# Kernel tuning notes

Hardware: AMD Instinct MI355X
Metric: run time of the kernel (lower is better)

The kernel has to match this reference:

```python
import jax, jax.numpy as jnp
import numpy as np

EPS = 1e-5

def binary_activation(x):
    # ReActNet piecewise-polynomial STE: forward = sign(x), grad follows poly
    m1 = (x < -1).astype(x.dtype)
    m2 = (x < 0).astype(x.dtype)
    m3 = (x < 1).astype(x.dtype)
    out1 = -1.0 * m1 + (x * x + 2.0 * x) * (1.0 - m1)
    out2 = out1 * m2 + (-x * x + 2.0 * x) * (1.0 - m2)
    out3 = out2 * m3 + 1.0 * (1.0 - m3)
    return jax.lax.stop_gradient(jnp.sign(x) - out3) + out3

def binary_conv(x, w, stride, padding):
    # per-output-channel scaled sign weights with clamp STE
    scale = jnp.mean(jnp.abs(w), axis=(1, 2, 3), keepdims=True)
    clipped = jnp.clip(w, -1.0, 1.0)
    bw = jax.lax.stop_gradient(scale * jnp.sign(w) - clipped) + clipped
    return jax.lax.conv_general_dilated(
        x, bw, window_strides=(stride, stride),
        padding=[(padding, padding), (padding, padding)],
        dimension_numbers=('NCHW', 'OIHW', 'NCHW'))

def batch_norm(x, g, b):
    mu = jnp.mean(x, axis=(0, 2, 3), keepdims=True)
    var = jnp.mean((x - mu) ** 2, axis=(0, 2, 3), keepdims=True)
    xn = (x - mu) * jax.lax.rsqrt(var + EPS)
    return xn * g[None, :, None, None] + b[None, :, None, None]

def prelu(x, a):
    a = a[None, :, None, None]
    return jnp.where(x >= 0, x, a * x)

def setup_inputs() -> dict:
    key = jax.random.key(0)
    ks = jax.random.split(key, 12)
    N, C, H, W = 32, 256, 56, 56
    d = {
        'x': jax.random.normal(ks[0], (N, C, H, W), jnp.float32),
        'b11': jax.random.normal(ks[1], (1, C, 1, 1), jnp.float32) * 0.1,
        'b12': jax.random.normal(ks[2], (1, C, 1, 1), jnp.float32) * 0.1,
        'b13': jax.random.normal(ks[3], (1, C, 1, 1), jnp.float32) * 0.1,
        'b21': jax.random.normal(ks[4], (1, C, 1, 1), jnp.float32) * 0.1,
        'b22': jax.random.normal(ks[5], (1, C, 1, 1), jnp.float32) * 0.1,
        'b23': jax.random.normal(ks[6], (1, C, 1, 1), jnp.float32) * 0.1,
        'w3x3': jax.random.normal(ks[7], (C, C, 3, 3), jnp.float32) * 0.05,
        'wpw': jax.random.normal(ks[8], (C, C, 1, 1), jnp.float32) * 0.05,
        'g1': jnp.ones((C,), jnp.float32),
        'be1': jnp.zeros((C,), jnp.float32),
        'g2': jnp.ones((C,), jnp.float32),
        'be2': jnp.zeros((C,), jnp.float32),
        'p1': jnp.full((C,), 0.25, jnp.float32),
        'p2': jnp.full((C,), 0.25, jnp.float32),
    }
    return d

def reference(x, b11, b12, b13, b21, b22, b23, w3x3, wpw, g1, be1, g2, be2, p1, p2):
    # stride=1, inplanes == planes branch
    out1 = binary_activation(x + b11)
    out1 = binary_conv(out1, w3x3, stride=1, padding=1)
    out1 = batch_norm(out1, g1, be1)
    out1 = x + out1
    out1 = prelu(out1 + b12, p1) + b13
    out2 = binary_activation(out1 + b21)
    out2 = binary_conv(out2, wpw, stride=1, padding=0)
    out2 = batch_norm(out2, g2, be2)
    out2 = out2 + out1
    out2 = prelu(out2 + b22, p2) + b23
    return out2
```

## Files before the change

### kernel.cpp

```cpp
#include <hip/hip_runtime.h>

typedef __attribute__((ext_vector_type(4))) float  f32x4;
typedef __attribute__((ext_vector_type(8))) short  s16x8;
typedef __attribute__((ext_vector_type(4))) int    i32x4;

#define MFMA16(a, b, c) __builtin_amdgcn_mfma_f32_16x16x32_bf16((a), (b), (c), 0, 0, 0)

__device__ __forceinline__ void gload_lds16(const void* g, void* l) {
  __builtin_amdgcn_global_load_lds((const __attribute__((address_space(1))) void*)g,
                                   (__attribute__((address_space(3))) void*)l, 16, 0, 0);
}

__device__ __forceinline__ unsigned short sgnbits(float v) {
  return v > 0.f ? (unsigned short)0x3F80u : (v < 0.f ? (unsigned short)0xBF80u : (unsigned short)0u);
}

__global__ __launch_bounds__(256) void prep_w(const float* __restrict__ w3,
                                              const float* __restrict__ wpw,
                                              unsigned short* __restrict__ w1s,
                                              unsigned short* __restrict__ w2s,
                                              float* __restrict__ scale1,
                                              float* __restrict__ scale2) {
  const int o = blockIdx.x;
  const int t = threadIdx.x;
  float s = 0.f;
  if (blockIdx.y == 0) {
    for (int u = t; u < 2304; u += 256) {
      int i = u / 9, tap = u % 9;
      float v = w3[(size_t)(o * 256 + i) * 9 + tap];
      s += fabsf(v);
      w1s[(size_t)(tap * 256 + o) * 256 + i] = sgnbits(v);
    }
  } else {
    float v = wpw[o * 256 + t];
    s = fabsf(v);
    w2s[o * 256 + t] = sgnbits(v);
  }
  for (int m = 1; m < 64; m <<= 1) s += __shfl_xor(s, m);
  __shared__ float red[4];
  if ((t & 63) == 0) red[t >> 6] = s;
  __syncthreads();
  if (t == 0) {
    float tot = red[0] + red[1] + red[2] + red[3];
    if (blockIdx.y == 0) scale1[o] = tot / 2304.f;
    else                 scale2[o] = tot / 256.f;
  }
}

__global__ __launch_bounds__(256) void sign_nhwc(const float* __restrict__ x,
                                                 const float* __restrict__ b11,
                                                 unsigned short* __restrict__ out) {
  __shared__ unsigned short l[56 * 256];
  __shared__ float cB[256];
  const int h = blockIdx.x, n = blockIdx.y, t = threadIdx.x;
  cB[t] = b11[t];
  __syncthreads();
  const int wv = t & 15, cg = t >> 4;
  if (wv < 14) {
    const int w0 = wv * 4;
    const int swz = (wv & 7) << 3;
#pragma unroll 4
    for (int it = 0; it < 16; ++it) {
      int c = it * 16 + cg;
      size_t idx = (size_t)(n * 256 + c) * 3136 + h * 56 + w0;
      f32x4 xv = *(const f32x4*)(x + idx);
      float bb = cB[c];
      int cs = c ^ swz;
      l[(w0 + 0) * 256 + cs] = sgnbits(xv[0] + bb);
      l[(w0 + 1) * 256 + cs] = sgnbits(xv[1] + bb);
      l[(w0 + 2) * 256 + cs] = sgnbits(xv[2] + bb);
      l[(w0 + 3) * 256 + cs] = sgnbits(xv[3] + bb);
    }
  }
  __syncthreads();
  unsigned short* op = out + ((size_t)(n * 56 + h) * 56) * 256;
  for (int u = t; u < 56 * 32; u += 256) {
    int w2 = u >> 5, cp = u & 31;
    *(i32x4*)(op + w2 * 256 + cp * 8) =
        *(const i32x4*)&l[w2 * 256 + ((cp * 8) ^ (((w2 >> 2) & 7) << 3))];
  }
}

template <int R>
__global__ __launch_bounds__(256, 2) void conv_bin(const unsigned short* __restrict__ sIn,
                                                   const unsigned short* __restrict__ wSgn,
                                                   float* __restrict__ raw,
                                                   float* __restrict__ S,
                                                   float* __restrict__ SS) {
  constexpr int KD   = 2 * R + 1;
  constexpr int TAPS = KD * KD;
  constexpr int ROWS = 4 + 2 * R;
  constexpr int COLS = 56 + 2 * R;
  __shared__ unsigned short lin[ROWS * COLS * 32];
  __shared__ unsigned short lw[TAPS * 64 * 32];

  const int ot = blockIdx.x, ht = blockIdx.y, n = blockIdx.z;
  const int h0 = ht * 4, oc0 = ot * 64;
  const int t = threadIdx.x;
  const int lane = t & 63, wv = t >> 6;
  const int wm = wv & 1, wn = wv >> 1;
  const int cl = lane & 15, kk = lane >> 4;

  for (int u = t; u < ROWS * COLS * 4; u += 256)
    *(i32x4*)((char*)lin + (size_t)u * 16) = (i32x4){0, 0, 0, 0};

  int bbase[7];
#pragma unroll
  for (int nf = 0; nf < 7; ++nf) {
    int pxl = (wn * 7 + nf) * 16 + cl;
    int r = pxl / 56, c = pxl % 56;
    bbase[nf] = (r * COLS + c) * 64 + kk * 16;
  }
  const int abase = (wm * 32 + cl) * 64 + kk * 16;

  f32x4 acc[2][7];
#pragma unroll
  for (int m = 0; m < 2; ++m)
#pragma unroll
    for (int nf = 0; nf < 7; ++nf) acc[m][nf] = (f32x4){0.f, 0.f, 0.f, 0.f};

  __syncthreads();

  for (int icc = 0; icc < 8; ++icc) {
#pragma unroll
    for (int rr = 0; rr < ROWS; ++rr) {
      int h = h0 - R + rr;
      if (h >= 0 && h < 56 && t < 224) {
        const char* src = (const char*)sIn +
            ((size_t)((n * 56 + h) * 56 + (t >> 2)) * 512 + icc * 64 + (t & 3) * 16);
        char* dst = (char*)lin + ((rr * COLS + R) * 64 + t * 16);
        gload_lds16(src, dst);
      }
    }
    for (int u = t; u < TAPS * 256; u += 256) {
      int tap = u >> 8, rest = u & 255;
      const char* src = (const char*)wSgn +
          ((size_t)(tap * 256 + oc0 + (rest >> 2)) * 512 + icc * 64 + (rest & 3) * 16);
      gload_lds16(src, (char*)lw + (size_t)u * 16);
    }
    __syncthreads();

#pragma unroll
    for (int kh = 0; kh < KD; ++kh)
#pragma unroll
      for (int kw = 0; kw < KD; ++kw) {
        const int tap = kh * KD + kw;
        s16x8 a0 = *(const s16x8*)((const char*)lw + (tap * 4096 + abase));
        s16x8 a1 = *(const s16x8*)((const char*)lw + (tap * 4096 + abase + 1024));
        const int toff = (kh * COLS + kw) * 64;
#pragma unroll
        for (int nf = 0; nf < 7; ++nf) {
          s16x8 b = *(const s16x8*)((const char*)lin + (bbase[nf] + toff));
          acc[0][nf] = MFMA16(a0, b, acc[0][nf]);
          acc[1][nf] = MFMA16(a1, b, acc[1][nf]);
        }
      }
    __syncthreads();
  }

  float sm[2][4], sq[2][4];
#pragma unroll
  for (int m = 0; m < 2; ++m)
#pragma unroll
    for (int r2 = 0; r2 < 4; ++r2) { sm[m][r2] = 0.f; sq[m][r2] = 0.f; }

  const size_t pbase = (size_t)n * 256 * 3136 + (size_t)h0 * 56;
#pragma unroll
  for (int m = 0; m < 2; ++m) {
    const int ocb = oc0 + wm * 32 + m * 16 + kk * 4;
#pragma unroll
    for (int nf = 0; nf < 7; ++nf) {
      const int pxl = (wn * 7 + nf) * 16 + cl;
      f32x4 v = acc[m][nf];
#pragma unroll
      for (int r2 = 0; r2 < 4; ++r2) {
        raw[pbase + (size_t)(ocb + r2) * 3136 + pxl] = v[r2];
        sm[m][r2] += v[r2];
        sq[m][r2] += v[r2] * v[r2];
      }
    }
  }
#pragma unroll
  for (int m = 0; m < 2; ++m)
#pragma unroll
    for (int r2 = 0; r2 < 4; ++r2) {
      float a = sm[m][r2], q = sq[m][r2];
      a += __shfl_xor(a, 1); q += __shfl_xor(q, 1);
      a += __shfl_xor(a, 2); q += __shfl_xor(q, 2);
      a += __shfl_xor(a, 4); q += __shfl_xor(q, 4);
      a += __shfl_xor(a, 8); q += __shfl_xor(q, 8);
      if (cl == 0) {
        int oc = oc0 + wm * 32 + m * 16 + kk * 4 + r2;
        atomicAdd(&S[oc], a);
        atomicAdd(&SS[oc], q);
      }
    }
}

__global__ void bn_coef(const float* __restrict__ S, const float* __restrict__ SS,
                        const float* __restrict__ scale, const float* __restrict__ g,
                        const float* __restrict__ be, const float* __restrict__ bext,
                        float* __restrict__ A, float* __restrict__ B) {
  int o = threadIdx.x;
  const float invN = 1.f / 100352.f;
  float mu_r  = S[o] * invN;
  float var_r = SS[o] * invN - mu_r * mu_r;
  float sc    = scale[o];
  float rstd  = rsqrtf(sc * sc * var_r + 1e-5f);
  A[o] = g[o] * rstd * sc;
  B[o] = be[o] - g[o] * rstd * sc * mu_r + bext[o];
}

__global__ __launch_bounds__(256) void mid_fuse(const float* __restrict__ raw,
                                                const float* __restrict__ x,
                                                const float* __restrict__ A1,
                                                const float* __restrict__ B1,
                                                const float* __restrict__ p1,
                                                const float* __restrict__ b13,
                                                const float* __restrict__ b21,
                                                float* __restrict__ t1,
                                                unsigned short* __restrict__ s2) {
  __shared__ unsigned short l[56 * 256];
  __shared__ float cA[256], cB[256], cP[256], cD[256], cE[256];
  const int h = blockIdx.x, n = blockIdx.y, t = threadIdx.x;
  cA[t] = A1[t]; cB[t] = B1[t]; cP[t] = p1[t]; cD[t] = b13[t]; cE[t] = b21[t];
  __syncthreads();
  const int wv = t & 15, cg = t >> 4;
  if (wv < 14) {
    const int w0 = wv * 4;
    const int swz = (wv & 7) << 3;
#pragma unroll 4
    for (int it = 0; it < 16; ++it) {
      int c = it * 16 + cg;
      size_t idx = (size_t)(n * 256 + c) * 3136 + h * 56 + w0;
      f32x4 xv = *(const f32x4*)(x + idx);
      f32x4 rv = *(const f32x4*)(raw + idx);
      float a = cA[c], b = cB[c], p = cP[c], d = cD[c], e = cE[c];
      f32x4 o;
      int cs = c ^ swz;
#pragma unroll
      for (int j = 0; j < 4; ++j) {
        float u = xv[j] + a * rv[j] + b;
        u = (u >= 0.f ? u : p * u) + d;
        o[j] = u;
        l[(w0 + j) * 256 + cs] = sgnbits(u + e);
      }
      *(f32x4*)(t1 + idx) = o;
    }
  }
  __syncthreads();
  unsigned short* op = s2 + ((size_t)(n * 56 + h) * 56) * 256;
  for (int u = t; u < 56 * 32; u += 256) {
    int w2 = u >> 5, cp = u & 31;
    *(i32x4*)(op + w2 * 256 + cp * 8) =
        *(const i32x4*)&l[w2 * 256 + ((cp * 8) ^ (((w2 >> 2) & 7) << 3))];
  }
}

__global__ __launch_bounds__(256) void final_fuse(const float* __restrict__ raw,
                                                  const float* __restrict__ A2,
                                                  const float* __restrict__ B2,
                                                  const float* __restrict__ p2,
                                                  const float* __restrict__ b23,
                                                  float* out) {
  const int c = blockIdx.x & 255;
  const size_t base = (size_t)blockIdx.x * 3136;
  const float a = A2[c], b = B2[c], p = p2[c], d = b23[c];
  for (int i = threadIdx.x; i < 784; i += 256) {
    f32x4 r  = *(const f32x4*)(raw + base + (size_t)i * 4);
    f32x4 tt = *(const f32x4*)(out + base + (size_t)i * 4);
    f32x4 o;
#pragma unroll
    for (int j = 0; j < 4; ++j) {
      float v = a * r[j] + b + tt[j];
      o[j] = (v >= 0.f ? v : p * v) + d;
    }
    *(f32x4*)(out + base + (size_t)i * 4) = o;
  }
}

extern "C" void kernel_launch(void* const* d_in, const int* in_sizes, int n_in,
                              void* d_out, int out_size, void* d_ws, size_t ws_size,
                              hipStream_t stream) {
  const float* x   = (const float*)d_in[0];
  const float* b11 = (const float*)d_in[1];
  const float* b12 = (const float*)d_in[2];
  const float* b13 = (const float*)d_in[3];
  const float* b21 = (const float*)d_in[4];
  const float* b22 = (const float*)d_in[5];
  const float* b23 = (const float*)d_in[6];
  const float* w3  = (const float*)d_in[7];
  const float* wpw = (const float*)d_in[8];
  const float* g1  = (const float*)d_in[9];
  const float* be1 = (const float*)d_in[10];
  const float* g2  = (const float*)d_in[11];
  const float* be2 = (const float*)d_in[12];
  const float* p1  = (const float*)d_in[13];
  const float* p2  = (const float*)d_in[14];

  char* ws = (char*)d_ws;
  float*          raw    = (float*)(ws);
  unsigned short* sgn    = (unsigned short*)(ws + 102760448);
  unsigned short* w1s    = (unsigned short*)(ws + 154140672);
  unsigned short* w2s    = (unsigned short*)(ws + 155320320);
  float*          scale1 = (float*)(ws + 155451392);
  float*          scale2 = (float*)(ws + 155452416);
  float*          S1     = (float*)(ws + 155453440);
  float*          SS1    = (float*)(ws + 155454464);
  float*          S2     = (float*)(ws + 155455488);
  float*          SS2    = (float*)(ws + 155456512);
  float*          A1     = (float*)(ws + 155457536);
  float*          B1     = (float*)(ws + 155458560);
  float*          A2     = (float*)(ws + 155459584);
  float*          B2     = (float*)(ws + 155460608);
  float*          t1     = (float*)d_out;

  hipMemsetAsync(ws + 155453440, 0, 4096, stream);

  prep_w<<<dim3(256, 2), 256, 0, stream>>>(w3, wpw, w1s, w2s, scale1, scale2);
  sign_nhwc<<<dim3(56, 32), 256, 0, stream>>>(x, b11, sgn);
  conv_bin<1><<<dim3(4, 14, 32), 256, 0, stream>>>(sgn, w1s, raw, S1, SS1);
  bn_coef<<<1, 256, 0, stream>>>(S1, SS1, scale1, g1, be1, b12, A1, B1);
  mid_fuse<<<dim3(56, 32), 256, 0, stream>>>(raw, x, A1, B1, p1, b13, b21, t1, sgn);
  conv_bin<0><<<dim3(4, 14, 32), 256, 0, stream>>>(sgn, w2s, raw, S2, SS2);
  bn_coef<<<1, 256, 0, stream>>>(S2, SS2, scale2, g2, be2, b22, A2, B2);
  final_fuse<<<dim3(8192), 256, 0, stream>>>(raw, A2, B2, p2, b23, (float*)d_out);
}
```

Measured before the change: 471.2 us.

## Split binary conv into specialized 3x3 and 1x1 kernels with int16 raw output

Replaces the templated conv with a dedicated 3x3 kernel (8-row tiles, 4x7 MFMA tiles per wave, XOR-swizzled LDS, remapped block order) and a 1x1 kernel treated as a GEMM over 112-pixel tiles with double-buffered staging across all 256 output channels. The raw conv outputs are stored as int16 instead of float32, since sign-times-sign dot products are integers bounded by 2304. This halves intermediate memory traffic in both the conv epilogue and the fused BN kernels. It adds more register pressure from the larger accumulator tile, and the block remapping assumes a fixed grid size.

```diff
diff --git a/kernel.cpp b/kernel.cpp
--- a/kernel.cpp
+++ b/kernel.cpp
@@ -2,6 +2,7 @@
 
 typedef __attribute__((ext_vector_type(4))) float  f32x4;
 typedef __attribute__((ext_vector_type(8))) short  s16x8;
+typedef __attribute__((ext_vector_type(4))) short  s16x4;
 typedef __attribute__((ext_vector_type(4))) int    i32x4;
 
 #define MFMA16(a, b, c) __builtin_amdgcn_mfma_f32_16x16x32_bf16((a), (b), (c), 0, 0, 0)
@@ -81,120 +82,209 @@
   }
 }
 
-template <int R>
-__global__ __launch_bounds__(256, 2) void conv_bin(const unsigned short* __restrict__ sIn,
-                                                   const unsigned short* __restrict__ wSgn,
-                                                   float* __restrict__ raw,
-                                                   float* __restrict__ S,
-                                                   float* __restrict__ SS) {
-  constexpr int KD   = 2 * R + 1;
-  constexpr int TAPS = KD * KD;
-  constexpr int ROWS = 4 + 2 * R;
-  constexpr int COLS = 56 + 2 * R;
-  __shared__ unsigned short lin[ROWS * COLS * 32];
-  __shared__ unsigned short lw[TAPS * 64 * 32];
-
-  const int ot = blockIdx.x, ht = blockIdx.y, n = blockIdx.z;
-  const int h0 = ht * 4, oc0 = ot * 64;
+__global__ __launch_bounds__(256, 2) void conv3x3(const unsigned short* __restrict__ sIn,
+                                                  const unsigned short* __restrict__ wSgn,
+                                                  short* __restrict__ raw,
+                                                  float* __restrict__ S,
+                                                  float* __restrict__ SS) {
+  __shared__ unsigned short lin[10 * 64 * 32];
+  __shared__ unsigned short lw[9 * 64 * 32];
+
+  int bid = (blockIdx.x & 7) * 112 + (blockIdx.x >> 3);
+  const int ot = bid & 3;
+  const int g  = bid >> 2;
+  const int ht = g % 7, n = g / 7;
+  const int h0 = ht * 8, oc0 = ot * 64;
+
   const int t = threadIdx.x;
   const int lane = t & 63, wv = t >> 6;
-  const int wm = wv & 1, wn = wv >> 1;
   const int cl = lane & 15, kk = lane >> 4;
-
-  for (int u = t; u < ROWS * COLS * 4; u += 256)
+  const int kswz = (kk ^ ((cl >> 1) & 3)) << 4;
+
+  for (int u = t; u < 10 * 64 * 4; u += 256)
     *(i32x4*)((char*)lin + (size_t)u * 16) = (i32x4){0, 0, 0, 0};
 
-  int bbase[7];
+  int q0[7];
 #pragma unroll
   for (int nf = 0; nf < 7; ++nf) {
-    int pxl = (wn * 7 + nf) * 16 + cl;
-    int r = pxl / 56, c = pxl % 56;
-    bbase[nf] = (r * COLS + c) * 64 + kk * 16;
-  }
-  const int abase = (wm * 32 + cl) * 64 + kk * 16;
-
-  f32x4 acc[2][7];
-#pragma unroll
-  for (int m = 0; m < 2; ++m)
+    int p = wv * 112 + nf * 16 + cl;
+    q0[nf] = (p / 56) * 64 + (p % 56);
+  }
+
+  f32x4 acc[4][7];
+#pragma unroll
+  for (int m = 0; m < 4; ++m)
 #pragma unroll
     for (int nf = 0; nf < 7; ++nf) acc[m][nf] = (f32x4){0.f, 0.f, 0.f, 0.f};
 
   __syncthreads();
 
   for (int icc = 0; icc < 8; ++icc) {
-#pragma unroll
-    for (int rr = 0; rr < ROWS; ++rr) {
-      int h = h0 - R + rr;
-      if (h >= 0 && h < 56 && t < 224) {
-        const char* src = (const char*)sIn +
-            ((size_t)((n * 56 + h) * 56 + (t >> 2)) * 512 + icc * 64 + (t & 3) * 16);
-        char* dst = (char*)lin + ((rr * COLS + R) * 64 + t * 16);
-        gload_lds16(src, dst);
-      }
-    }
-    for (int u = t; u < TAPS * 256; u += 256) {
-      int tap = u >> 8, rest = u & 255;
-      const char* src = (const char*)wSgn +
-          ((size_t)(tap * 256 + oc0 + (rest >> 2)) * 512 + icc * 64 + (rest & 3) * 16);
+    if (t < 224) {
+      const int pw = t >> 2, sl = t & 3;
+      const int srcslot = sl ^ (((1 + pw) >> 1) & 3);
+#pragma unroll
+      for (int rr = 0; rr < 10; ++rr) {
+        int h = h0 - 1 + rr;
+        if (h >= 0 && h < 56) {
+          const char* src = (const char*)sIn +
+              ((size_t)((n * 56 + h) * 56 + pw) * 512 + icc * 64 + srcslot * 16);
+          char* dst = (char*)lin + ((rr * 64 + 1) * 64 + t * 16);
+          gload_lds16(src, dst);
+        }
+      }
+    }
+#pragma unroll
+    for (int i = 0; i < 9; ++i) {
+      int u = i * 256 + t;
+      int tap = u >> 8, oc_e = (u >> 2) & 63;
+      int srcslot = (u & 3) ^ ((u >> 3) & 3);
+      const unsigned short* src = wSgn +
+          ((size_t)(tap * 256 + oc0 + oc_e) * 256 + icc * 32 + srcslot * 8);
       gload_lds16(src, (char*)lw + (size_t)u * 16);
     }
     __syncthreads();
 
 #pragma unroll
-    for (int kh = 0; kh < KD; ++kh)
-#pragma unroll
-      for (int kw = 0; kw < KD; ++kw) {
-        const int tap = kh * KD + kw;
-        s16x8 a0 = *(const s16x8*)((const char*)lw + (tap * 4096 + abase));
-        s16x8 a1 = *(const s16x8*)((const char*)lw + (tap * 4096 + abase + 1024));
-        const int toff = (kh * COLS + kw) * 64;
+    for (int kh = 0; kh < 3; ++kh)
+#pragma unroll
+      for (int kw = 0; kw < 3; ++kw) {
+        const int tap = kh * 3 + kw;
+        s16x8 a[4];
+#pragma unroll
+        for (int m = 0; m < 4; ++m)
+          a[m] = *(const s16x8*)((const char*)lw + (tap * 64 + m * 16 + cl) * 64 + kswz);
 #pragma unroll
         for (int nf = 0; nf < 7; ++nf) {
-          s16x8 b = *(const s16x8*)((const char*)lin + (bbase[nf] + toff));
-          acc[0][nf] = MFMA16(a0, b, acc[0][nf]);
-          acc[1][nf] = MFMA16(a1, b, acc[1][nf]);
+          int qq = q0[nf] + kw;
+          int addr = (qq + kh * 64) * 64 + ((kk ^ ((qq >> 1) & 3)) << 4);
+          s16x8 b = *(const s16x8*)((const char*)lin + addr);
+#pragma unroll
+          for (int m = 0; m < 4; ++m) acc[m][nf] = MFMA16(a[m], b, acc[m][nf]);
         }
       }
     __syncthreads();
   }
 
-  float sm[2][4], sq[2][4];
-#pragma unroll
-  for (int m = 0; m < 2; ++m)
-#pragma unroll
-    for (int r2 = 0; r2 < 4; ++r2) { sm[m][r2] = 0.f; sq[m][r2] = 0.f; }
-
-  const size_t pbase = (size_t)n * 256 * 3136 + (size_t)h0 * 56;
-#pragma unroll
-  for (int m = 0; m < 2; ++m) {
-    const int ocb = oc0 + wm * 32 + m * 16 + kk * 4;
+#pragma unroll
+  for (int m = 0; m < 4; ++m) {
+    float sm[4] = {0.f, 0.f, 0.f, 0.f}, sq[4] = {0.f, 0.f, 0.f, 0.f};
 #pragma unroll
     for (int nf = 0; nf < 7; ++nf) {
-      const int pxl = (wn * 7 + nf) * 16 + cl;
+      int p = wv * 112 + nf * 16 + cl;
+      int h = h0 + p / 56, w = p % 56;
+      size_t base = ((size_t)n * 256 + oc0 + m * 16 + kk * 4) * 3136 + h * 56 + w;
       f32x4 v = acc[m][nf];
 #pragma unroll
       for (int r2 = 0; r2 < 4; ++r2) {
-        raw[pbase + (size_t)(ocb + r2) * 3136 + pxl] = v[r2];
-        sm[m][r2] += v[r2];
-        sq[m][r2] += v[r2] * v[r2];
-      }
-    }
-  }
-#pragma unroll
-  for (int m = 0; m < 2; ++m)
+        raw[base + (size_t)r2 * 3136] = (short)(int)v[r2];
+        sm[r2] += v[r2];
+        sq[r2] += v[r2] * v[r2];
+      }
+    }
 #pragma unroll
     for (int r2 = 0; r2 < 4; ++r2) {
-      float a = sm[m][r2], q = sq[m][r2];
-      a += __shfl_xor(a, 1); q += __shfl_xor(q, 1);
-      a += __shfl_xor(a, 2); q += __shfl_xor(q, 2);
-      a += __shfl_xor(a, 4); q += __shfl_xor(q, 4);
-      a += __shfl_xor(a, 8); q += __shfl_xor(q, 8);
+      float aa = sm[r2], qq = sq[r2];
+      aa += __shfl_xor(aa, 1); qq += __shfl_xor(qq, 1);
+      aa += __shfl_xor(aa, 2); qq += __shfl_xor(qq, 2);
+      aa += __shfl_xor(aa, 4); qq += __shfl_xor(qq, 4);
+      aa += __shfl_xor(aa, 8); qq += __shfl_xor(qq, 8);
       if (cl == 0) {
-        int oc = oc0 + wm * 32 + m * 16 + kk * 4 + r2;
-        atomicAdd(&S[oc], a);
-        atomicAdd(&SS[oc], q);
-      }
-    }
+        int oc = oc0 + m * 16 + kk * 4 + r2;
+        atomicAdd(&S[oc], aa);
+        atomicAdd(&SS[oc], qq);
+      }
+    }
+  }
+}
+
+__global__ __launch_bounds__(256, 2) void conv1x1(const unsigned short* __restrict__ sIn,
+                                                  const unsigned short* __restrict__ wSgn,
+                                                  short* __restrict__ raw,
+                                                  float* __restrict__ S,
+                                                  float* __restrict__ SS) {
+  __shared__ unsigned short lin[2 * 112 * 32];
+  __shared__ unsigned short lw[2 * 256 * 32];
+
+  const int b = blockIdx.x;
+  const int n = b / 28;
+  const int hw0 = (b % 28) * 112;
+  const size_t px0 = (size_t)n * 3136 + hw0;
+  const int t = threadIdx.x, lane = t & 63, wv = t >> 6;
+  const int cl = lane & 15, kk = lane >> 4;
+  const int kswz = (kk ^ ((cl >> 1) & 3)) << 4;
+
+#define STAGE_1x1(icc, bufi)                                                        \
+  {                                                                                 \
+    for (int u = t; u < 448; u += 256) {                                            \
+      int srcslot = (u & 3) ^ ((u >> 3) & 3);                                       \
+      const char* src = (const char*)sIn +                                          \
+          ((px0 + (u >> 2)) * 512 + (icc) * 64 + srcslot * 16);                     \
+      gload_lds16(src, (char*)lin + (bufi) * 7168 + u * 16);                        \
+    }                                                                               \
+    _Pragma("unroll")                                                               \
+    for (int i = 0; i < 4; ++i) {                                                   \
+      int u = i * 256 + t;                                                          \
+      int srcslot = (u & 3) ^ ((u >> 3) & 3);                                       \
+      const unsigned short* src = wSgn +                                            \
+          ((size_t)(u >> 2) * 256 + (icc) * 32 + srcslot * 8);                      \
+      gload_lds16(src, (char*)lw + (bufi) * 16384 + u * 16);                        \
+    }                                                                               \
+  }
+
+  f32x4 acc[4][7];
+#pragma unroll
+  for (int m = 0; m < 4; ++m)
+#pragma unroll
+    for (int nf = 0; nf < 7; ++nf) acc[m][nf] = (f32x4){0.f, 0.f, 0.f, 0.f};
+
+  STAGE_1x1(0, 0);
+  __syncthreads();
+  for (int icc = 0; icc < 8; ++icc) {
+    const int cur = icc & 1;
+    if (icc < 7) STAGE_1x1(icc + 1, cur ^ 1);
+    s16x8 bfr[7];
+#pragma unroll
+    for (int nf = 0; nf < 7; ++nf)
+      bfr[nf] = *(const s16x8*)((const char*)lin + cur * 7168 + (nf * 16 + cl) * 64 + kswz);
+#pragma unroll
+    for (int m = 0; m < 4; ++m) {
+      s16x8 a = *(const s16x8*)((const char*)lw + cur * 16384 +
+                                (wv * 64 + m * 16 + cl) * 64 + kswz);
+#pragma unroll
+      for (int nf = 0; nf < 7; ++nf) acc[m][nf] = MFMA16(a, bfr[nf], acc[m][nf]);
+    }
+    __syncthreads();
+  }
+
+#pragma unroll
+  for (int m = 0; m < 4; ++m) {
+    float sm[4] = {0.f, 0.f, 0.f, 0.f}, sq[4] = {0.f, 0.f, 0.f, 0.f};
+    size_t base0 = ((size_t)n * 256 + wv * 64 + m * 16 + kk * 4) * 3136 + hw0;
+#pragma unroll
+    for (int nf = 0; nf < 7; ++nf) {
+      f32x4 v = acc[m][nf];
+#pragma unroll
+      for (int r2 = 0; r2 < 4; ++r2) {
+        raw[base0 + (size_t)r2 * 3136 + nf * 16 + cl] = (short)(int)v[r2];
+        sm[r2] += v[r2];
+        sq[r2] += v[r2] * v[r2];
+      }
+    }
+#pragma unroll
+    for (int r2 = 0; r2 < 4; ++r2) {
+      float aa = sm[r2], qq = sq[r2];
+      aa += __shfl_xor(aa, 1); qq += __shfl_xor(qq, 1);
+      aa += __shfl_xor(aa, 2); qq += __shfl_xor(qq, 2);
+      aa += __shfl_xor(aa, 4); qq += __shfl_xor(qq, 4);
+      aa += __shfl_xor(aa, 8); qq += __shfl_xor(qq, 8);
+      if (cl == 0) {
+        int oc = wv * 64 + m * 16 + kk * 4 + r2;
+        atomicAdd(&S[oc], aa);
+        atomicAdd(&SS[oc], qq);
+      }
+    }
+  }
 }
 
 __global__ void bn_coef(const float* __restrict__ S, const float* __restrict__ SS,
@@ -211,7 +301,7 @@
   B[o] = be[o] - g[o] * rstd * sc * mu_r + bext[o];
 }
 
-__global__ __launch_bounds__(256) void mid_fuse(const float* __restrict__ raw,
+__global__ __launch_bounds__(256) void mid_fuse(const short* __restrict__ raw,
                                                 const float* __restrict__ x,
                                                 const float* __restrict__ A1,
                                                 const float* __restrict__ B1,
@@ -234,13 +324,13 @@
       int c = it * 16 + cg;
       size_t idx = (size_t)(n * 256 + c) * 3136 + h * 56 + w0;
       f32x4 xv = *(const f32x4*)(x + idx);
-      f32x4 rv = *(const f32x4*)(raw + idx);
+      s16x4 rv = *(const s16x4*)(raw + idx);
       float a = cA[c], b = cB[c], p = cP[c], d = cD[c], e = cE[c];
       f32x4 o;
       int cs = c ^ swz;
 #pragma unroll
       for (int j = 0; j < 4; ++j) {
-        float u = xv[j] + a * rv[j] + b;
+        float u = xv[j] + a * (float)rv[j] + b;
         u = (u >= 0.f ? u : p * u) + d;
         o[j] = u;
         l[(w0 + j) * 256 + cs] = sgnbits(u + e);
@@ -257,7 +347,7 @@
   }
 }
 
-__global__ __launch_bounds__(256) void final_fuse(const float* __restrict__ raw,
+__global__ __launch_bounds__(256) void final_fuse(const short* __restrict__ raw,
                                                   const float* __restrict__ A2,
                                                   const float* __restrict__ B2,
                                                   const float* __restrict__ p2,
@@ -267,12 +357,12 @@
   const size_t base = (size_t)blockIdx.x * 3136;
   const float a = A2[c], b = B2[c], p = p2[c], d = b23[c];
   for (int i = threadIdx.x; i < 784; i += 256) {
-    f32x4 r  = *(const f32x4*)(raw + base + (size_t)i * 4);
+    s16x4 r  = *(const s16x4*)(raw + base + (size_t)i * 4);
     f32x4 tt = *(const f32x4*)(out + base + (size_t)i * 4);
     f32x4 o;
 #pragma unroll
     for (int j = 0; j < 4; ++j) {
-      float v = a * r[j] + b + tt[j];
+      float v = a * (float)r[j] + b + tt[j];
       o[j] = (v >= 0.f ? v : p * v) + d;
     }
     *(f32x4*)(out + base + (size_t)i * 4) = o;
@@ -299,30 +389,30 @@
   const float* p2  = (const float*)d_in[14];
 
   char* ws = (char*)d_ws;
-  float*          raw    = (float*)(ws);
-  unsigned short* sgn    = (unsigned short*)(ws + 102760448);
-  unsigned short* w1s    = (unsigned short*)(ws + 154140672);
-  unsigned short* w2s    = (unsigned short*)(ws + 155320320);
-  float*          scale1 = (float*)(ws + 155451392);
-  float*          scale2 = (float*)(ws + 155452416);
-  float*          S1     = (float*)(ws + 155453440);
-  float*          SS1    = (float*)(ws + 155454464);
-  float*          S2     = (float*)(ws + 155455488);
-  float*          SS2    = (float*)(ws + 155456512);
-  float*          A1     = (float*)(ws + 155457536);
-  float*          B1     = (float*)(ws + 155458560);
-  float*          A2     = (float*)(ws + 155459584);
-  float*          B2     = (float*)(ws + 155460608);
+  short*          raw    = (short*)(ws);
+  unsigned short* sgn    = (unsigned short*)(ws + 51380224);
+  unsigned short* w1s    = (unsigned short*)(ws + 102760448);
+  unsigned short* w2s    = (unsigned short*)(ws + 103940096);
+  float*          scale1 = (float*)(ws + 104071168);
+  float*          scale2 = (float*)(ws + 104072192);
+  float*          S1     = (float*)(ws + 104073216);
+  float*          SS1    = (float*)(ws + 104074240);
+  float*          S2     = (float*)(ws + 104075264);
+  float*          SS2    = (float*)(ws + 104076288);
+  float*          A1     = (float*)(ws + 104077312);
+  float*          B1     = (float*)(ws + 104078336);
+  float*          A2     = (float*)(ws + 104079360);
+  float*          B2     = (float*)(ws + 104080384);
   float*          t1     = (float*)d_out;
 
-  hipMemsetAsync(ws + 155453440, 0, 4096, stream);
+  hipMemsetAsync(ws + 104073216, 0, 4096, stream);
 
   prep_w<<<dim3(256, 2), 256, 0, stream>>>(w3, wpw, w1s, w2s, scale1, scale2);
   sign_nhwc<<<dim3(56, 32), 256, 0, stream>>>(x, b11, sgn);
-  conv_bin<1><<<dim3(4, 14, 32), 256, 0, stream>>>(sgn, w1s, raw, S1, SS1);
+  conv3x3<<<dim3(896), 256, 0, stream>>>(sgn, w1s, raw, S1, SS1);
   bn_coef<<<1, 256, 0, stream>>>(S1, SS1, scale1, g1, be1, b12, A1, B1);
   mid_fuse<<<dim3(56, 32), 256, 0, stream>>>(raw, x, A1, B1, p1, b13, b21, t1, sgn);
-  conv_bin<0><<<dim3(4, 14, 32), 256, 0, stream>>>(sgn, w2s, raw, S2, SS2);
+  conv1x1<<<dim3(896), 256, 0, stream>>>(sgn, w2s, raw, S2, SS2);
   bn_coef<<<1, 256, 0, stream>>>(S2, SS2, scale2, g2, be2, b22, A2, B2);
   final_fuse<<<dim3(8192), 256, 0, stream>>>(raw, A2, B2, p2, b23, (float*)d_out);
 }
```

Result: faster. 434.4 us (-7.8%).
